# Kernel tuning notes

Measured on AMD Instinct MI355X. Metric: run time of the kernel, lower is better.

Reference implementation:

```python
import jax, jax.numpy as jnp
import numpy as np

D = 768

def setup_inputs() -> dict:
    key = jax.random.key(0)
    k1, k2, k3, k4, k5 = jax.random.split(key, 5)
    B, C, Q = 32, 512, 128
    cont_embs = jax.random.normal(k1, (B, C, D), dtype=jnp.float32)
    ques_embs = jax.random.normal(k2, (B, Q, D), dtype=jnp.float32)
    cont_masks = jax.random.randint(k3, (B, C), 0, 2, dtype=jnp.int32)
    ques_masks = jax.random.randint(k4, (B, Q), 0, 2, dtype=jnp.int32)
    # S_W param, 'uniform' initializer (keras default: U[-0.05, 0.05])
    S_W = jax.random.uniform(k5, (3 * D,), dtype=jnp.float32, minval=-0.05, maxval=0.05)
    return {"cont_embs": cont_embs, "cont_masks": cont_masks,
            "ques_embs": ques_embs, "ques_masks": ques_masks, "S_W": S_W}

def reference(cont_embs, cont_masks, ques_embs, ques_masks, S_W):
    c, q = cont_embs, ques_embs          # (B,C,D), (B,Q,D)
    # Decompose reduce_sum(concat([c_tile, q_tile, c*q], -1) * S_W, -1)
    # into rank-1 bias terms + a single matmul (no (B,C,Q,3D) materialization).
    w1, w2, w3 = S_W[:D], S_W[D:2 * D], S_W[2 * D:]
    similarity = (jnp.einsum('bcd,d->bc', c, w1)[:, :, None]
                  + jnp.einsum('bqd,d->bq', q, w2)[:, None, :]
                  + jnp.einsum('bcd,bqd->bcq', c * w3, q))   # (B,C,Q)
    NEG = jnp.float32(-1e30)
    exp_mask_c2q = (1.0 - ques_masks.astype(jnp.float32))[:, None, :] * NEG  # (B,1,Q)
    # NOTE: original code applies softmax over axis=1 (context axis), faithfully kept.
    c2q_dist = jax.nn.softmax(similarity + exp_mask_c2q, axis=1)  # (B,C,Q)
    c2q = jnp.einsum('bcq,bqd->bcd', c2q_dist, q)                 # (B,C,D)
    S_max = jnp.max(similarity, axis=2)                           # (B,C)
    exp_mask_S = (1.0 - cont_masks.astype(jnp.float32)) * NEG     # (B,C)
    c_dash_dist = jax.nn.softmax(S_max + exp_mask_S, axis=1)      # (B,C)
    c_dash = jnp.einsum('bc,bcd->bd', c_dash_dist, c)[:, None, :] # (B,1,D)
    c_c2q = c * c2q
    c_c_dash = c * c_dash
    attn_output = jnp.concatenate([c2q, c_c2q, c_c_dash], axis=2)  # (B,C,3D)
    # dropout omitted (deterministic reference)
    blended_reps = jnp.concatenate([c, attn_output], axis=2)       # (B,C,4D)
    return blended_reps
```

## Files before the change

kernel.cpp:

```cpp
#include <hip/hip_runtime.h>
#include <hip/hip_bf16.h>

#define B_ 32
#define C_ 512
#define Q_ 128
#define D_ 768
constexpr float NEGV = -1e30f;
constexpr float CINV = 1.0f / 512.0f;

typedef short bf16x8 __attribute__((ext_vector_type(8)));
typedef short bf16x4 __attribute__((ext_vector_type(4)));
typedef float f32x4 __attribute__((ext_vector_type(4)));

__device__ __forceinline__ short f2bf(float x) {
    union { float f; unsigned u; } v; v.f = x;
    unsigned r = v.u + 0x7fffu + ((v.u >> 16) & 1u);
    return (short)(r >> 16);
}

__global__ void k_prep(const float* __restrict__ cont, const float* __restrict__ ques,
                       const float* __restrict__ SW, short* __restrict__ contw3,
                       short* __restrict__ quesbf, float* __restrict__ cdot,
                       float* __restrict__ qdot) {
    int lane = threadIdx.x & 63;
    int r = blockIdx.x * 4 + (threadIdx.x >> 6);
    float acc = 0.f;
    if (r < B_ * C_) {
        const float* row = cont + (size_t)r * D_;
        short* orow = contw3 + (size_t)r * D_;
#pragma unroll
        for (int i = 0; i < 3; ++i) {
            int k = i * 256 + lane * 4;
            float4 f = *(const float4*)(row + k);
            float4 a = *(const float4*)(SW + k);
            float4 m = *(const float4*)(SW + 2 * D_ + k);
            acc += f.x * a.x + f.y * a.y + f.z * a.z + f.w * a.w;
            bf16x4 p;
            p[0] = f2bf(f.x * m.x); p[1] = f2bf(f.y * m.y);
            p[2] = f2bf(f.z * m.z); p[3] = f2bf(f.w * m.w);
            *(bf16x4*)(orow + k) = p;
        }
#pragma unroll
        for (int off = 32; off; off >>= 1) acc += __shfl_xor(acc, off, 64);
        if (lane == 0) cdot[r] = acc;
    } else {
        int r2 = r - B_ * C_;
        const float* row = ques + (size_t)r2 * D_;
        short* orow = quesbf + (size_t)r2 * D_;
#pragma unroll
        for (int i = 0; i < 3; ++i) {
            int k = i * 256 + lane * 4;
            float4 f = *(const float4*)(row + k);
            float4 a = *(const float4*)(SW + D_ + k);
            acc += f.x * a.x + f.y * a.y + f.z * a.z + f.w * a.w;
            bf16x4 p;
            p[0] = f2bf(f.x); p[1] = f2bf(f.y); p[2] = f2bf(f.z); p[3] = f2bf(f.w);
            *(bf16x4*)(orow + k) = p;
        }
#pragma unroll
        for (int off = 32; off; off >>= 1) acc += __shfl_xor(acc, off, 64);
        if (lane == 0) qdot[r2] = acc;
    }
}

__global__ void k_qt(const short* __restrict__ quesbf, short* __restrict__ quesT) {
    const int d0 = blockIdx.x * 64, q0 = blockIdx.y * 64, b = blockIdx.z;
    __shared__ short T[64][65];
    const int t = threadIdx.x;
#pragma unroll
    for (int p = 0; p < 2; ++p) {
        int ql = p * 32 + (t >> 3), dl = (t & 7) * 8;
        bf16x8 v = *(const bf16x8*)(quesbf + ((size_t)(b * Q_ + q0 + ql)) * D_ + d0 + dl);
#pragma unroll
        for (int j = 0; j < 8; ++j) T[ql][dl + j] = v[j];
    }
    __syncthreads();
#pragma unroll
    for (int p = 0; p < 2; ++p) {
        int dl = p * 32 + (t >> 3), ql = (t & 7) * 8;
        bf16x8 v;
#pragma unroll
        for (int j = 0; j < 8; ++j) v[j] = T[ql + j][dl];
        *(bf16x8*)(quesT + ((size_t)(b * D_ + d0 + dl)) * Q_ + q0 + ql) = v;
    }
}

__global__ void __launch_bounds__(256) k_sim(const short* __restrict__ contw3,
                                             const short* __restrict__ quesbf,
                                             const float* __restrict__ cdot,
                                             const float* __restrict__ qdot,
                                             float* __restrict__ S,
                                             float* __restrict__ Smax) {
    const int b = blockIdx.y, c0 = blockIdx.x * 32;
    const int t = threadIdx.x, w = t >> 6, l = t & 63;
    const int llo = l & 15, lhi = l >> 4;
    __shared__ float rowpart[4][32];
    const short* Ab = contw3 + ((size_t)(b * C_ + c0)) * D_ + lhi * 8;
    const short* Bb = quesbf + ((size_t)(b * Q_ + w * 32)) * D_ + lhi * 8;
    f32x4 acc[2][2] = {};
#pragma unroll 4
    for (int k0 = 0; k0 < D_; k0 += 32) {
        bf16x8 a0 = *(const bf16x8*)(Ab + (size_t)llo * D_ + k0);
        bf16x8 a1 = *(const bf16x8*)(Ab + (size_t)(16 + llo) * D_ + k0);
        bf16x8 b0 = *(const bf16x8*)(Bb + (size_t)llo * D_ + k0);
        bf16x8 b1 = *(const bf16x8*)(Bb + (size_t)(16 + llo) * D_ + k0);
        acc[0][0] = __builtin_amdgcn_mfma_f32_16x16x32_bf16(a0, b0, acc[0][0], 0, 0, 0);
        acc[0][1] = __builtin_amdgcn_mfma_f32_16x16x32_bf16(a0, b1, acc[0][1], 0, 0, 0);
        acc[1][0] = __builtin_amdgcn_mfma_f32_16x16x32_bf16(a1, b0, acc[1][0], 0, 0, 0);
        acc[1][1] = __builtin_amdgcn_mfma_f32_16x16x32_bf16(a1, b1, acc[1][1], 0, 0, 0);
    }
    float qd0 = qdot[b * Q_ + w * 32 + llo];
    float qd1 = qdot[b * Q_ + w * 32 + 16 + llo];
#pragma unroll
    for (int mi = 0; mi < 2; ++mi) {
#pragma unroll
        for (int i = 0; i < 4; ++i) {
            int cl = mi * 16 + lhi * 4 + i;
            float cd = cdot[b * C_ + c0 + cl];
            size_t srow = ((size_t)(b * C_ + c0 + cl)) * Q_;
            float v0 = acc[mi][0][i] + cd + qd0;
            float v1 = acc[mi][1][i] + cd + qd1;
            S[srow + w * 32 + llo] = v0;
            S[srow + w * 32 + 16 + llo] = v1;
            float vm = fmaxf(v0, v1);
#pragma unroll
            for (int off = 1; off < 16; off <<= 1) vm = fmaxf(vm, __shfl_xor(vm, off, 64));
            if (llo == 0) rowpart[w][cl] = vm;
        }
    }
    __syncthreads();
    if (t < 32)
        Smax[b * C_ + c0 + t] = fmaxf(fmaxf(rowpart[0][t], rowpart[1][t]),
                                      fmaxf(rowpart[2][t], rowpart[3][t]));
}

__global__ void k_colstats(const float* __restrict__ S, const int* __restrict__ qmask,
                           float* __restrict__ colM, float* __restrict__ scl) {
    const int b = blockIdx.y;
    const int ql = threadIdx.x & 15, q = blockIdx.x * 16 + ql;
    const int strip = threadIdx.x >> 4;
    float m = -INFINITY, lsum = 0.f;
    const float* Sp = S + ((size_t)(b * C_ + strip * 32)) * Q_ + q;
    for (int c = 0; c < 32; ++c) {
        float v = Sp[(size_t)c * Q_];
        if (v > m) { lsum = lsum * __expf(m - v) + 1.f; m = v; }
        else lsum += __expf(v - m);
    }
    __shared__ float sm[16][16], sl[16][16];
    sm[strip][ql] = m; sl[strip][ql] = lsum;
    __syncthreads();
    if (threadIdx.x < 16) {
        float M = sm[0][ql], L = sl[0][ql];
#pragma unroll
        for (int i = 1; i < 16; ++i) {
            float mi = sm[i][ql], li = sl[i][ql];
            if (mi > M) { L = L * __expf(M - mi) + li; M = mi; }
            else L += li * __expf(mi - M);
        }
        colM[b * Q_ + q] = M;
        scl[b * Q_ + q] = qmask[b * Q_ + q] ? 1.f / L : -1.f;
    }
}

__global__ void k_dist(const float* __restrict__ S, const float* __restrict__ colM,
                       const float* __restrict__ scl, short* __restrict__ distbf) {
    const int r = blockIdx.x * 16 + (threadIdx.x >> 4);
    const int b = r >> 9;
    const int q8 = (threadIdx.x & 15) * 8;
    const float* sp = S + (size_t)r * Q_ + q8;
    float4 s0 = *(const float4*)sp;
    float4 s1 = *(const float4*)(sp + 4);
    float4 m0 = *(const float4*)(colM + b * Q_ + q8);
    float4 m1 = *(const float4*)(colM + b * Q_ + q8 + 4);
    float4 c0 = *(const float4*)(scl + b * Q_ + q8);
    float4 c1 = *(const float4*)(scl + b * Q_ + q8 + 4);
    float sv[8] = {s0.x, s0.y, s0.z, s0.w, s1.x, s1.y, s1.z, s1.w};
    float mv[8] = {m0.x, m0.y, m0.z, m0.w, m1.x, m1.y, m1.z, m1.w};
    float cv[8] = {c0.x, c0.y, c0.z, c0.w, c1.x, c1.y, c1.z, c1.w};
    bf16x8 o;
#pragma unroll
    for (int j = 0; j < 8; ++j)
        o[j] = f2bf(cv[j] < 0.f ? CINV : __expf(sv[j] - mv[j]) * cv[j]);
    *(bf16x8*)(distbf + (size_t)r * Q_ + q8) = o;
}

__global__ void k_cdash(const float* __restrict__ cont, const int* __restrict__ cmask,
                        const float* __restrict__ Smax, float* __restrict__ cdash) {
    int b = blockIdx.y, d0 = blockIdx.x * 64;
    __shared__ float dist[C_];
    __shared__ float red[256];
    __shared__ float ps[4][64];
    int t = threadIdx.x;
    float v0 = Smax[b * C_ + t]       + (cmask[b * C_ + t]       ? 0.f : NEGV);
    float v1 = Smax[b * C_ + t + 256] + (cmask[b * C_ + t + 256] ? 0.f : NEGV);
    float m = fmaxf(v0, v1);
    red[t] = m; __syncthreads();
    for (int s = 128; s; s >>= 1) { if (t < s) red[t] = fmaxf(red[t], red[t + s]); __syncthreads(); }
    m = red[0]; __syncthreads();
    float e0 = __expf(v0 - m), e1 = __expf(v1 - m);
    red[t] = e0 + e1; __syncthreads();
    for (int s = 128; s; s >>= 1) { if (t < s) red[t] += red[t + s]; __syncthreads(); }
    float inv = 1.f / red[0];
    dist[t] = e0 * inv; dist[t + 256] = e1 * inv;
    __syncthreads();
    int d = d0 + (t & 63), strip = t >> 6;
    float acc = 0.f;
    const float* cp = cont + ((size_t)(b * C_ + strip * 128)) * D_ + d;
#pragma unroll 8
    for (int c = 0; c < 128; ++c) acc += dist[strip * 128 + c] * cp[(size_t)c * D_];
    ps[strip][t & 63] = acc;
    __syncthreads();
    if (t < 64) cdash[b * D_ + d0 + t] = ps[0][t] + ps[1][t] + ps[2][t] + ps[3][t];
}

__global__ void __launch_bounds__(256) k_final(const float* __restrict__ cont,
                                               const short* __restrict__ distbf,
                                               const short* __restrict__ quesT,
                                               const float* __restrict__ cdash,
                                               float* __restrict__ out) {
    const int b = blockIdx.z, c0 = blockIdx.x * 64, D0 = blockIdx.y * 64;
    const int t = threadIdx.x, w = t >> 6, l = t & 63;
    const int woffm = (w >> 1) * 32, woffn = (w & 1) * 32;
    const int llo = l & 15, lhi = l >> 4;
    __shared__ float Cf[64][68];
    const short* Ab = distbf + ((size_t)(b * C_ + c0 + woffm)) * Q_ + lhi * 8;
    const short* Bb = quesT + ((size_t)(b * D_ + D0 + woffn)) * Q_ + lhi * 8;
    f32x4 acc[2][2] = {};
#pragma unroll
    for (int kk = 0; kk < 4; ++kk) {
        const int k0 = kk * 32;
        bf16x8 a0 = *(const bf16x8*)(Ab + llo * Q_ + k0);
        bf16x8 a1 = *(const bf16x8*)(Ab + (16 + llo) * Q_ + k0);
        bf16x8 b0 = *(const bf16x8*)(Bb + llo * Q_ + k0);
        bf16x8 b1 = *(const bf16x8*)(Bb + (16 + llo) * Q_ + k0);
        acc[0][0] = __builtin_amdgcn_mfma_f32_16x16x32_bf16(a0, b0, acc[0][0], 0, 0, 0);
        acc[0][1] = __builtin_amdgcn_mfma_f32_16x16x32_bf16(a0, b1, acc[0][1], 0, 0, 0);
        acc[1][0] = __builtin_amdgcn_mfma_f32_16x16x32_bf16(a1, b0, acc[1][0], 0, 0, 0);
        acc[1][1] = __builtin_amdgcn_mfma_f32_16x16x32_bf16(a1, b1, acc[1][1], 0, 0, 0);
    }
#pragma unroll
    for (int mi = 0; mi < 2; ++mi)
#pragma unroll
        for (int ni = 0; ni < 2; ++ni)
#pragma unroll
            for (int i = 0; i < 4; ++i)
                Cf[woffm + mi * 16 + lhi * 4 + i][woffn + ni * 16 + llo] = acc[mi][ni][i];
    __syncthreads();
    const int col = (t & 15) * 4;
    const float4 dv = *(const float4*)(cdash + b * D_ + D0 + col);
#pragma unroll
    for (int p = 0; p < 4; ++p) {
        int r = p * 16 + (t >> 4);
        float4 av = *(const float4*)&Cf[r][col];
        const float* cp = cont + ((size_t)(b * C_ + c0 + r)) * D_ + D0 + col;
        float4 cv = *(const float4*)cp;
        float4 m1 = {cv.x * av.x, cv.y * av.y, cv.z * av.z, cv.w * av.w};
        float4 m2 = {cv.x * dv.x, cv.y * dv.y, cv.z * dv.z, cv.w * dv.w};
        float* op = out + ((size_t)(b * C_ + c0 + r)) * (size_t)(4 * D_) + D0 + col;
        *(float4*)op = cv;
        *(float4*)(op + D_) = av;
        *(float4*)(op + 2 * D_) = m1;
        *(float4*)(op + 3 * D_) = m2;
    }
}

extern "C" void kernel_launch(void* const* d_in, const int* in_sizes, int n_in,
                              void* d_out, int out_size, void* d_ws, size_t ws_size,
                              hipStream_t stream) {
    const float* cont  = (const float*)d_in[0];
    const int*   cmask = (const int*)d_in[1];
    const float* ques  = (const float*)d_in[2];
    const int*   qmask = (const int*)d_in[3];
    const float* SW    = (const float*)d_in[4];
    float* out = (float*)d_out;

    float* ws      = (float*)d_ws;
    float* S       = ws;
    float* Smax    = S + (size_t)B_ * C_ * Q_;
    float* colM    = Smax + B_ * C_;
    float* scl     = colM + B_ * Q_;
    float* cdot    = scl + B_ * Q_;
    float* qdot    = cdot + B_ * C_;
    float* cdash   = qdot + B_ * Q_;
    short* contw3  = (short*)(cdash + B_ * D_);
    short* quesbf  = contw3 + (size_t)B_ * C_ * D_;
    short* quesT   = quesbf + (size_t)B_ * Q_ * D_;
    short* distbf  = quesT + (size_t)B_ * D_ * Q_;

    k_prep<<<(B_ * C_ + B_ * Q_) / 4, 256, 0, stream>>>(cont, ques, SW, contw3, quesbf, cdot, qdot);
    k_qt<<<dim3(D_ / 64, Q_ / 64, B_), 256, 0, stream>>>(quesbf, quesT);
    k_sim<<<dim3(C_ / 32, B_), 256, 0, stream>>>(contw3, quesbf, cdot, qdot, S, Smax);
    k_colstats<<<dim3(Q_ / 16, B_), 256, 0, stream>>>(S, qmask, colM, scl);
    k_dist<<<B_ * C_ / 16, 256, 0, stream>>>(S, colM, scl, distbf);
    k_cdash<<<dim3(D_ / 64, B_), 256, 0, stream>>>(cont, cmask, Smax, cdash);
    k_final<<<dim3(C_ / 64, D_ / 64, B_), 256, 0, stream>>>(cont, distbf, quesT, cdash, out);
}
```

Baseline: 322.2 us.

## Fuse column softmax, c_dash and q transpose into one mid kernel; nontemporal output stores

Merges k_colstats, k_dist, k_cdash and k_qt into a single heterogeneous kernel k_mid, with blocks split by blockIdx.x range. The column-softmax blocks now compute stats and write the bf16 distribution directly, which removes the colM/scl round trip and several launches. k_final writes its large output with nontemporal stores to reduce cache pollution. The trade-off is a small grid for the softmax part (8×32 blocks, each walking 16 columns with strided reads) and uneven work across the merged block types.

```diff
diff --git a/kernel.cpp b/kernel.cpp
--- a/kernel.cpp
+++ b/kernel.cpp
@@ -16,6 +16,11 @@
     union { float f; unsigned u; } v; v.f = x;
     unsigned r = v.u + 0x7fffu + ((v.u >> 16) & 1u);
     return (short)(r >> 16);
+}
+
+__device__ __forceinline__ void nt_store4(float* p, float x, float y, float z, float w) {
+    f32x4 v = {x, y, z, w};
+    __builtin_nontemporal_store(v, (f32x4*)p);
 }
 
 __global__ void k_prep(const float* __restrict__ cont, const float* __restrict__ ques,
@@ -60,28 +65,6 @@
 #pragma unroll
         for (int off = 32; off; off >>= 1) acc += __shfl_xor(acc, off, 64);
         if (lane == 0) qdot[r2] = acc;
-    }
-}
-
-__global__ void k_qt(const short* __restrict__ quesbf, short* __restrict__ quesT) {
-    const int d0 = blockIdx.x * 64, q0 = blockIdx.y * 64, b = blockIdx.z;
-    __shared__ short T[64][65];
-    const int t = threadIdx.x;
-#pragma unroll
-    for (int p = 0; p < 2; ++p) {
-        int ql = p * 32 + (t >> 3), dl = (t & 7) * 8;
-        bf16x8 v = *(const bf16x8*)(quesbf + ((size_t)(b * Q_ + q0 + ql)) * D_ + d0 + dl);
-#pragma unroll
-        for (int j = 0; j < 8; ++j) T[ql][dl + j] = v[j];
-    }
-    __syncthreads();
-#pragma unroll
-    for (int p = 0; p < 2; ++p) {
-        int dl = p * 32 + (t >> 3), ql = (t & 7) * 8;
-        bf16x8 v;
-#pragma unroll
-        for (int j = 0; j < 8; ++j) v[j] = T[ql + j][dl];
-        *(bf16x8*)(quesT + ((size_t)(b * D_ + d0 + dl)) * Q_ + q0 + ql) = v;
     }
 }
 
@@ -134,83 +117,97 @@
                                       fmaxf(rowpart[2][t], rowpart[3][t]));
 }
 
-__global__ void k_colstats(const float* __restrict__ S, const int* __restrict__ qmask,
-                           float* __restrict__ colM, float* __restrict__ scl) {
+__global__ void __launch_bounds__(256) k_mid(const float* __restrict__ S,
+                                             const int* __restrict__ qmask,
+                                             const float* __restrict__ cont,
+                                             const int* __restrict__ cmask,
+                                             const float* __restrict__ Smax,
+                                             const short* __restrict__ quesbf,
+                                             short* __restrict__ distbf,
+                                             float* __restrict__ cdash,
+                                             short* __restrict__ quesT) {
     const int b = blockIdx.y;
-    const int ql = threadIdx.x & 15, q = blockIdx.x * 16 + ql;
-    const int strip = threadIdx.x >> 4;
-    float m = -INFINITY, lsum = 0.f;
-    const float* Sp = S + ((size_t)(b * C_ + strip * 32)) * Q_ + q;
-    for (int c = 0; c < 32; ++c) {
-        float v = Sp[(size_t)c * Q_];
-        if (v > m) { lsum = lsum * __expf(m - v) + 1.f; m = v; }
-        else lsum += __expf(v - m);
-    }
-    __shared__ float sm[16][16], sl[16][16];
-    sm[strip][ql] = m; sl[strip][ql] = lsum;
-    __syncthreads();
-    if (threadIdx.x < 16) {
-        float M = sm[0][ql], L = sl[0][ql];
-#pragma unroll
-        for (int i = 1; i < 16; ++i) {
-            float mi = sm[i][ql], li = sl[i][ql];
-            if (mi > M) { L = L * __expf(M - mi) + li; M = mi; }
-            else L += li * __expf(mi - M);
-        }
-        colM[b * Q_ + q] = M;
-        scl[b * Q_ + q] = qmask[b * Q_ + q] ? 1.f / L : -1.f;
-    }
-}
-
-__global__ void k_dist(const float* __restrict__ S, const float* __restrict__ colM,
-                       const float* __restrict__ scl, short* __restrict__ distbf) {
-    const int r = blockIdx.x * 16 + (threadIdx.x >> 4);
-    const int b = r >> 9;
-    const int q8 = (threadIdx.x & 15) * 8;
-    const float* sp = S + (size_t)r * Q_ + q8;
-    float4 s0 = *(const float4*)sp;
-    float4 s1 = *(const float4*)(sp + 4);
-    float4 m0 = *(const float4*)(colM + b * Q_ + q8);
-    float4 m1 = *(const float4*)(colM + b * Q_ + q8 + 4);
-    float4 c0 = *(const float4*)(scl + b * Q_ + q8);
-    float4 c1 = *(const float4*)(scl + b * Q_ + q8 + 4);
-    float sv[8] = {s0.x, s0.y, s0.z, s0.w, s1.x, s1.y, s1.z, s1.w};
-    float mv[8] = {m0.x, m0.y, m0.z, m0.w, m1.x, m1.y, m1.z, m1.w};
-    float cv[8] = {c0.x, c0.y, c0.z, c0.w, c1.x, c1.y, c1.z, c1.w};
-    bf16x8 o;
-#pragma unroll
-    for (int j = 0; j < 8; ++j)
-        o[j] = f2bf(cv[j] < 0.f ? CINV : __expf(sv[j] - mv[j]) * cv[j]);
-    *(bf16x8*)(distbf + (size_t)r * Q_ + q8) = o;
-}
-
-__global__ void k_cdash(const float* __restrict__ cont, const int* __restrict__ cmask,
-                        const float* __restrict__ Smax, float* __restrict__ cdash) {
-    int b = blockIdx.y, d0 = blockIdx.x * 64;
-    __shared__ float dist[C_];
-    __shared__ float red[256];
-    __shared__ float ps[4][64];
-    int t = threadIdx.x;
-    float v0 = Smax[b * C_ + t]       + (cmask[b * C_ + t]       ? 0.f : NEGV);
-    float v1 = Smax[b * C_ + t + 256] + (cmask[b * C_ + t + 256] ? 0.f : NEGV);
-    float m = fmaxf(v0, v1);
-    red[t] = m; __syncthreads();
-    for (int s = 128; s; s >>= 1) { if (t < s) red[t] = fmaxf(red[t], red[t + s]); __syncthreads(); }
-    m = red[0]; __syncthreads();
-    float e0 = __expf(v0 - m), e1 = __expf(v1 - m);
-    red[t] = e0 + e1; __syncthreads();
-    for (int s = 128; s; s >>= 1) { if (t < s) red[t] += red[t + s]; __syncthreads(); }
-    float inv = 1.f / red[0];
-    dist[t] = e0 * inv; dist[t + 256] = e1 * inv;
-    __syncthreads();
-    int d = d0 + (t & 63), strip = t >> 6;
-    float acc = 0.f;
-    const float* cp = cont + ((size_t)(b * C_ + strip * 128)) * D_ + d;
+    const int t = threadIdx.x;
+    if (blockIdx.x < 8) {
+        const int q0 = blockIdx.x * 16;
+        const int ql = t & 15, strip = t >> 4;
+        __shared__ float sm[16][16], sl[16][16];
+        __shared__ float colMl[16], scll[16];
+        float m = -INFINITY, lsum = 0.f;
+        const float* Sp = S + ((size_t)(b * C_ + strip * 32)) * Q_ + q0 + ql;
+        for (int c = 0; c < 32; ++c) {
+            float v = Sp[(size_t)c * Q_];
+            if (v > m) { lsum = lsum * __expf(m - v) + 1.f; m = v; }
+            else lsum += __expf(v - m);
+        }
+        sm[strip][ql] = m; sl[strip][ql] = lsum;
+        __syncthreads();
+        if (t < 16) {
+            float M = sm[0][t], L = sl[0][t];
+#pragma unroll
+            for (int i = 1; i < 16; ++i) {
+                float mi = sm[i][t], li = sl[i][t];
+                if (mi > M) { L = L * __expf(M - mi) + li; M = mi; }
+                else L += li * __expf(mi - M);
+            }
+            colMl[t] = M;
+            scll[t] = qmask[b * Q_ + q0 + t] ? 1.f / L : -1.f;
+        }
+        __syncthreads();
+        const float cm = colMl[ql], sc = scll[ql];
+        short* dp = distbf + ((size_t)(b * C_ + strip * 32)) * Q_ + q0 + ql;
+#pragma unroll 4
+        for (int c = 0; c < 32; ++c) {
+            float v = Sp[(size_t)c * Q_];
+            float dist = (sc < 0.f) ? CINV : __expf(v - cm) * sc;
+            dp[(size_t)c * Q_] = f2bf(dist);
+        }
+    } else if (blockIdx.x < 20) {
+        const int d0 = (blockIdx.x - 8) * 64;
+        __shared__ float dist[C_];
+        __shared__ float red[256];
+        __shared__ float ps[4][64];
+        float v0 = Smax[b * C_ + t]       + (cmask[b * C_ + t]       ? 0.f : NEGV);
+        float v1 = Smax[b * C_ + t + 256] + (cmask[b * C_ + t + 256] ? 0.f : NEGV);
+        float m = fmaxf(v0, v1);
+        red[t] = m; __syncthreads();
+        for (int s = 128; s; s >>= 1) { if (t < s) red[t] = fmaxf(red[t], red[t + s]); __syncthreads(); }
+        m = red[0]; __syncthreads();
+        float e0 = __expf(v0 - m), e1 = __expf(v1 - m);
+        red[t] = e0 + e1; __syncthreads();
+        for (int s = 128; s; s >>= 1) { if (t < s) red[t] += red[t + s]; __syncthreads(); }
+        float inv = 1.f / red[0];
+        dist[t] = e0 * inv; dist[t + 256] = e1 * inv;
+        __syncthreads();
+        int d = d0 + (t & 63), strip = t >> 6;
+        float acc = 0.f;
+        const float* cp = cont + ((size_t)(b * C_ + strip * 128)) * D_ + d;
 #pragma unroll 8
-    for (int c = 0; c < 128; ++c) acc += dist[strip * 128 + c] * cp[(size_t)c * D_];
-    ps[strip][t & 63] = acc;
-    __syncthreads();
-    if (t < 64) cdash[b * D_ + d0 + t] = ps[0][t] + ps[1][t] + ps[2][t] + ps[3][t];
+        for (int c = 0; c < 128; ++c) acc += dist[strip * 128 + c] * cp[(size_t)c * D_];
+        ps[strip][t & 63] = acc;
+        __syncthreads();
+        if (t < 64) cdash[b * D_ + d0 + t] = ps[0][t] + ps[1][t] + ps[2][t] + ps[3][t];
+    } else {
+        const int tx = blockIdx.x - 20;
+        const int d0 = (tx % 12) * 64, q0 = (tx / 12) * 64;
+        __shared__ short T[64][65];
+#pragma unroll
+        for (int p = 0; p < 2; ++p) {
+            int ql = p * 32 + (t >> 3), dl = (t & 7) * 8;
+            bf16x8 v = *(const bf16x8*)(quesbf + ((size_t)(b * Q_ + q0 + ql)) * D_ + d0 + dl);
+#pragma unroll
+            for (int j = 0; j < 8; ++j) T[ql][dl + j] = v[j];
+        }
+        __syncthreads();
+#pragma unroll
+        for (int p = 0; p < 2; ++p) {
+            int dl = p * 32 + (t >> 3), ql = (t & 7) * 8;
+            bf16x8 v;
+#pragma unroll
+            for (int j = 0; j < 8; ++j) v[j] = T[ql + j][dl];
+            *(bf16x8*)(quesT + ((size_t)(b * D_ + d0 + dl)) * Q_ + q0 + ql) = v;
+        }
+    }
 }
 
 __global__ void __launch_bounds__(256) k_final(const float* __restrict__ cont,
@@ -254,13 +251,11 @@
         float4 av = *(const float4*)&Cf[r][col];
         const float* cp = cont + ((size_t)(b * C_ + c0 + r)) * D_ + D0 + col;
         float4 cv = *(const float4*)cp;
-        float4 m1 = {cv.x * av.x, cv.y * av.y, cv.z * av.z, cv.w * av.w};
-        float4 m2 = {cv.x * dv.x, cv.y * dv.y, cv.z * dv.z, cv.w * dv.w};
         float* op = out + ((size_t)(b * C_ + c0 + r)) * (size_t)(4 * D_) + D0 + col;
-        *(float4*)op = cv;
-        *(float4*)(op + D_) = av;
-        *(float4*)(op + 2 * D_) = m1;
-        *(float4*)(op + 3 * D_) = m2;
+        nt_store4(op, cv.x, cv.y, cv.z, cv.w);
+        nt_store4(op + D_, av.x, av.y, av.z, av.w);
+        nt_store4(op + 2 * D_, cv.x * av.x, cv.y * av.y, cv.z * av.z, cv.w * av.w);
+        nt_store4(op + 3 * D_, cv.x * dv.x, cv.y * dv.y, cv.z * dv.z, cv.w * dv.w);
     }
 }
 
@@ -277,9 +272,7 @@
     float* ws      = (float*)d_ws;
     float* S       = ws;
     float* Smax    = S + (size_t)B_ * C_ * Q_;
-    float* colM    = Smax + B_ * C_;
-    float* scl     = colM + B_ * Q_;
-    float* cdot    = scl + B_ * Q_;
+    float* cdot    = Smax + B_ * C_;
     float* qdot    = cdot + B_ * C_;
     float* cdash   = qdot + B_ * Q_;
     short* contw3  = (short*)(cdash + B_ * D_);
@@ -288,10 +281,7 @@
     short* distbf  = quesT + (size_t)B_ * D_ * Q_;
 
     k_prep<<<(B_ * C_ + B_ * Q_) / 4, 256, 0, stream>>>(cont, ques, SW, contw3, quesbf, cdot, qdot);
-    k_qt<<<dim3(D_ / 64, Q_ / 64, B_), 256, 0, stream>>>(quesbf, quesT);
     k_sim<<<dim3(C_ / 32, B_), 256, 0, stream>>>(contw3, quesbf, cdot, qdot, S, Smax);
-    k_colstats<<<dim3(Q_ / 16, B_), 256, 0, stream>>>(S, qmask, colM, scl);
-    k_dist<<<B_ * C_ / 16, 256, 0, stream>>>(S, colM, scl, distbf);
-    k_cdash<<<dim3(D_ / 64, B_), 256, 0, stream>>>(cont, cmask, Smax, cdash);
+    k_mid<<<dim3(44, B_), 256, 0, stream>>>(S, qmask, cont, cmask, Smax, quesbf, distbf, cdash, quesT);
     k_final<<<dim3(C_ / 64, D_ / 64, B_), 256, 0, stream>>>(cont, distbf, quesT, cdash, out);
 }
```

Measured after the change: 321.6 us. Within noise of the previous version (-0.2%).
